# Optimization experiments

Measured on AMD Instinct MI355X. Metric: run time of the kernel, lower is better.

The kernel has to match this reference:

```python
import jax, jax.numpy as jnp
import numpy as np

B = 8192
H_IN = 128
H = 512
Z = 128
N = 512   # must equal H due to W_up(h,h) -> W_down(n,.) chaining in the source
RW = 16
TEMP = 0.666
EPS = 1e-20


def _xavier(key, shape):
    fan_in, fan_out = shape[0], shape[1]
    lim = float(np.sqrt(6.0 / (fan_in + fan_out)))
    return jax.random.uniform(key, shape, jnp.float32, -lim, lim)


def setup_inputs() -> dict:
    key = jax.random.key(0)
    ks = jax.random.split(key, 24)
    inp = {
        'latent': jax.random.normal(ks[0], (B, Z), jnp.float32),
        'inputs': jnp.zeros((B, H_IN), jnp.float32),
        'gumbel_u': jax.random.uniform(ks[1], (RW, B, N), jnp.float32),
        # weights stored [in, out] for x @ W
        'W_int': _xavier(ks[2], (Z, H)),   'b_int': jnp.zeros((H,), jnp.float32),
        'W_intl': _xavier(ks[3], (Z, H)),  'b_intl': jnp.zeros((H,), jnp.float32),
        'W_hup': _xavier(ks[4], (H, H)),   'b_hup': jnp.zeros((H,), jnp.float32),
        'W_cup': _xavier(ks[5], (H, H)),   'b_cup': jnp.zeros((H,), jnp.float32),
        'W_hupl': _xavier(ks[6], (H, H)),  'b_hupl': jnp.zeros((H,), jnp.float32),
        'W_cupl': _xavier(ks[7], (H, H)),  'b_cupl': jnp.zeros((H,), jnp.float32),
        'W_lstm': _xavier(ks[8], (H_IN + H, 4 * H)), 'b_lstm': jnp.zeros((4 * H,), jnp.float32),
        'W_up': _xavier(ks[9], (H, H)),    'b_up': jnp.zeros((H,), jnp.float32),
        'W_down': _xavier(ks[10], (N, H_IN)),        # no bias
        'W_downl': _xavier(ks[11], (N, H_IN)),       # no bias
        'W_outl': _xavier(ks[12], (H, 1)), 'b_outl': jnp.zeros((1,), jnp.float32),
    }
    return inp


def _lstm_step(x, hx, cx, W_lstm, b_lstm):
    gates = jnp.concatenate([x, hx], axis=1) @ W_lstm + b_lstm  # [B, 4H]
    i, g, f, o = jnp.split(gates, 4, axis=1)
    cy = cx * jax.nn.sigmoid(f + 1.0) + jax.nn.sigmoid(i) * jnp.tanh(g)
    hy = jax.nn.sigmoid(o) * jnp.tanh(cy)
    return hy, cy


def _forward(latent, inputs, gumbel_u,
             W_int, b_int, W_intl, b_intl,
             W_hup, b_hup, W_cup, b_cup,
             W_hupl, b_hupl, W_cupl, b_cupl,
             W_lstm, b_lstm, W_up, b_up,
             W_down, W_downl, W_outl, b_outl):
    inter = jnp.tanh(latent @ W_int + b_int)
    hx = jnp.tanh(inter @ W_hup + b_hup)
    cx = jnp.tanh(inter @ W_cup + b_cup)
    inter_l = jnp.tanh(latent @ W_intl + b_intl)
    hxl = jnp.tanh(inter_l @ W_hupl + b_hupl)
    cxl = jnp.tanh(inter_l @ W_cupl + b_cupl)

    def step1(carry, u):
        x, h, c = carry
        hy, cy = _lstm_step(x, h, c, W_lstm, b_lstm)
        logits = hy @ W_up + b_up                       # [B, N]
        g = -jnp.log(-jnp.log(u + EPS) + EPS)           # gumbel noise
        y = jax.nn.softmax((logits + g) / TEMP, axis=1)
        y_hard = (y == jnp.max(y, axis=1, keepdims=True)).astype(y.dtype)
        y = jax.lax.stop_gradient(y_hard - y) + y       # straight-through hard sample
        return (y @ W_down, hy, cy), y

    _, out_steps = jax.lax.scan(step1, (inputs, hx, cx), gumbel_u)  # [RW, B, N]

    def step2(carry, y):
        h, c = carry
        xl = y @ W_downl
        hy, cy = _lstm_step(xl, h, c, W_lstm, b_lstm)   # source reuses lstm_cell here
        return (hy, cy), hy @ W_outl + b_outl           # [B, 1]

    _, line_steps = jax.lax.scan(step2, (hxl, cxl), out_steps)      # [RW, B, 1]

    return (jnp.transpose(out_steps, (1, 0, 2)),   # [B, RW, N]
            jnp.transpose(line_steps, (1, 0, 2)))  # [B, RW, 1]


def reference(latent, inputs, gumbel_u,
              W_int, b_int, W_intl, b_intl,
              W_hup, b_hup, W_cup, b_cup,
              W_hupl, b_hupl, W_cupl, b_cupl,
              W_lstm, b_lstm, W_up, b_up,
              W_down, W_downl, W_outl, b_outl):
    return _forward(latent, inputs, gumbel_u,
                    W_int, b_int, W_intl, b_intl,
                    W_hup, b_hup, W_cup, b_cup,
                    W_hupl, b_hupl, W_cupl, b_cupl,
                    W_lstm, b_lstm, W_up, b_up,
                    W_down, W_downl, W_outl, b_outl)
```

## Files before the change

### kernel.cpp

```cpp
#include <hip/hip_runtime.h>

#define NB 8192
#define NH 512
#define NZ 128
#define NIN 128
#define NN 512
#define NRW 16
#define NG 2048

typedef _Float16 f16;
typedef _Float16 f16x8 __attribute__((ext_vector_type(8)));
typedef float f32x4 __attribute__((ext_vector_type(4)));

__device__ __forceinline__ float sigm(float x) { return 1.0f / (1.0f + expf(-x)); }

__device__ __forceinline__ int oc_of(int c)
{
    return (((c >> 4) & 3) << 9) + ((c >> 6) << 4) + (c & 15);
}
__device__ __forceinline__ int cperm(int j)
{
    return (j & 15) | (((j >> 4) & 31) << 6) | (((j >> 9) & 3) << 4);
}

__device__ __forceinline__ void swz_xcd(int& bx, int& by)
{
    const int gx = gridDim.x;
    const int nwg = gx * gridDim.y;
    int lin = by * gx + bx;
    lin = (lin & 7) * (nwg >> 3) + (lin >> 3);
    const int sh = 31 - __clz(gx);
    bx = lin & (gx - 1);
    by = lin >> sh;
}

__device__ __forceinline__ void gload16(const f16* g, f16* l)
{
    __builtin_amdgcn_global_load_lds(
        (const __attribute__((address_space(1))) void*)g,
        (__attribute__((address_space(3))) void*)l, 16, 0, 0);
}

__device__ __forceinline__ int swz4(int row) { return (row & 3) ^ ((row >> 2) & 3); }

__device__ __forceinline__ void stage_tile(f16* tilebase, const f16* src,
                                           int rowbase, int kb, int wid, int lane)
{
#pragma unroll
    for (int q = 0; q < 2; ++q) {
        const int iw = wid * 2 + q;
        const int chunk = (iw << 6) | lane;
        const int row = chunk >> 2;
        const int p = (chunk & 3) ^ swz4(row);
        const f16* g = src + (size_t)(rowbase + row) * NH + kb + (p << 3);
        gload16(g, tilebase + (iw << 9));
    }
}

__device__ __forceinline__ f16x8 frag(const f16* tile, int row, int sl)
{
    return *(const f16x8*)(tile + row * 32 + ((sl ^ swz4(row)) << 3));
}

__device__ __forceinline__ void readA(f16x8 (&a)[4], const f16* sbuf, int wr, int r16, int sl)
{
#pragma unroll
    for (int f = 0; f < 4; ++f) a[f] = frag(sbuf, wr + f * 16 + r16, sl);
}

__device__ __forceinline__ void loadBfr(f16x8 (&d)[4], const f16* p, size_t base)
{
#pragma unroll
    for (int f = 0; f < 4; ++f) d[f] = *(const f16x8*)(p + base + f * 512);
}

__device__ __forceinline__ f32x4 MM(const f16x8 a, const f16x8 b, f32x4 c)
{
    return __builtin_amdgcn_mfma_f32_16x16x32_f16(a, b, c, 0, 0, 0);
}

template<int SPLIT>
__device__ __forceinline__ void core3(const f16* Ahi, const f16* Alo,
                                      const f16* Bph, const f16* Bpl,
                                      f16* s0h, f16* s0l, f16* s1h, f16* s1l,
                                      int bm, int bnblk, int wid, int lane, int wr, int wc2,
                                      f32x4 (&acc)[4][4])
{
    const int r16 = lane & 15, sl = lane >> 4;
    const size_t bwoff = (size_t)(wc2 << 11) + lane * 8;
    f16x8 bAh[4], bAl[4], bBh[4], bBl[4];

    stage_tile(s0h, Ahi, bm, 0, wid, lane);
    if (SPLIT) stage_tile(s0l, Alo, bm, 0, wid, lane);
    loadBfr(bAh, Bph, (((size_t)bnblk << 4) << 12) + bwoff);
    if (SPLIT) loadBfr(bAl, Bpl, (((size_t)bnblk << 4) << 12) + bwoff);

#pragma unroll 1
    for (int kt = 0; kt < 16; kt += 2) {
        __syncthreads();
        {
            const int kn = kt + 1;
            stage_tile(s1h, Ahi, bm, kn << 5, wid, lane);
            if (SPLIT) stage_tile(s1l, Alo, bm, kn << 5, wid, lane);
            loadBfr(bBh, Bph, ((((size_t)bnblk << 4) + kn) << 12) + bwoff);
            if (SPLIT) loadBfr(bBl, Bpl, ((((size_t)bnblk << 4) + kn) << 12) + bwoff);
        }
        f16x8 ah[4], al[4];
        readA(ah, s0h, wr, r16, sl);
        if (SPLIT) readA(al, s0l, wr, r16, sl);
        __builtin_amdgcn_s_setprio(1);
#pragma unroll
        for (int i = 0; i < 4; ++i)
#pragma unroll
            for (int j = 0; j < 4; ++j) {
                acc[i][j] = MM(ah[i], bAh[j], acc[i][j]);
                if (SPLIT) {
                    acc[i][j] = MM(al[i], bAh[j], acc[i][j]);
                    acc[i][j] = MM(ah[i], bAl[j], acc[i][j]);
                }
            }
        __builtin_amdgcn_s_setprio(0);
        __syncthreads();
        if (kt + 2 < 16) {
            const int kn = kt + 2;
            stage_tile(s0h, Ahi, bm, kn << 5, wid, lane);
            if (SPLIT) stage_tile(s0l, Alo, bm, kn << 5, wid, lane);
            loadBfr(bAh, Bph, ((((size_t)bnblk << 4) + kn) << 12) + bwoff);
            if (SPLIT) loadBfr(bAl, Bpl, ((((size_t)bnblk << 4) + kn) << 12) + bwoff);
        }
        readA(ah, s1h, wr, r16, sl);
        if (SPLIT) readA(al, s1l, wr, r16, sl);
        __builtin_amdgcn_s_setprio(1);
#pragma unroll
        for (int i = 0; i < 4; ++i)
#pragma unroll
            for (int j = 0; j < 4; ++j) {
                acc[i][j] = MM(ah[i], bBh[j], acc[i][j]);
                if (SPLIT) {
                    acc[i][j] = MM(al[i], bBh[j], acc[i][j]);
                    acc[i][j] = MM(ah[i], bBl[j], acc[i][j]);
                }
            }
        __builtin_amdgcn_s_setprio(0);
    }
}

template<int DO_L1, int DO_L2>
__global__ __launch_bounds__(256, 2)
void fused_gate(const f16* __restrict__ a1hi, const f16* __restrict__ a1lo,
                const f16* __restrict__ a2hi,
                const f16* __restrict__ Wlp_hi, const f16* __restrict__ Wlp_lo,
                const float* __restrict__ blp,
                const float* __restrict__ gdown, const float* __restrict__ gdownl,
                const float2* __restrict__ part,
                float* __restrict__ out0, int t_out,
                float* __restrict__ c1, f16* __restrict__ o1hi, f16* __restrict__ o1lo,
                float* __restrict__ c2, f16* __restrict__ o2hi,
                const float* __restrict__ Woutl, float* __restrict__ out1, int t2)
{
    __shared__ f16 s[4][4096];
    __shared__ int winlds[128];
    int bx = blockIdx.x, by = blockIdx.y;
    swz_xcd(bx, by);
    const int bm = by << 7;
    const int tid = threadIdx.x;
    const int wid = tid >> 6, lane = tid & 63;
    const int wr = ((wid >> 1) & 1) << 6;
    const int wc2 = wid & 1;
    const bool isL1 = DO_L1 && (!DO_L2 || blockIdx.z == 0);

    if (part != nullptr && tid < 128) {
        const float2* p = part + (size_t)(bm + tid) * 8;
        float best = -INFINITY;
        int bi = 0x7fffffff;
#pragma unroll
        for (int q = 0; q < 8; ++q) {
            const float2 pv = p[q];
            if (pv.x > best || (pv.x == best && (int)pv.y < bi)) { best = pv.x; bi = (int)pv.y; }
        }
        winlds[tid] = bi;
    }

    f32x4 acc[4][4];
#pragma unroll
    for (int i = 0; i < 4; ++i)
#pragma unroll
        for (int j = 0; j < 4; ++j) acc[i][j] = (f32x4)(0.0f);

    const int m = lane & 15, rg = lane >> 4;
    const int colb = (bx << 7) + (wc2 << 6);
    const int jj = ((colb >> 6) << 4) + m;
    float bi4[4];
#pragma unroll
    for (int g = 0; g < 4; ++g) bi4[g] = blp[colb + g * 16 + m];

    if (isL1) {
        core3<1>(a1hi, a1lo, Wlp_hi, Wlp_lo, s[0], s[1], s[2], s[3],
                 bm, bx, wid, lane, wr, wc2, acc);
#pragma unroll
        for (int i = 0; i < 4; ++i) {
#pragma unroll
            for (int r = 0; r < 4; ++r) {
                const int row = bm + wr + i * 16 + rg * 4 + r;
                float ex[4] = {0.f, 0.f, 0.f, 0.f};
                if (part != nullptr) {
                    const float* exr = gdown + (size_t)winlds[row - bm] * NG;
#pragma unroll
                    for (int g = 0; g < 4; ++g) ex[g] = exr[colb + g * 16 + m];
                }
                const float ig = acc[i][0][r] + bi4[0] + ex[0];
                const float gg = acc[i][1][r] + bi4[1] + ex[1];
                const float fg = acc[i][2][r] + bi4[2] + ex[2];
                const float og = acc[i][3][r] + bi4[3] + ex[3];
                const size_t cidx = (size_t)row * NH + jj;
                const float cx = c1[cidx];
                const float cy = cx * sigm(fg + 1.0f) + sigm(ig) * tanhf(gg);
                const float hy = sigm(og) * tanhf(cy);
                c1[cidx] = cy;
                const f16 a = (f16)hy;
                o1hi[cidx] = a;
                o1lo[cidx] = (f16)(hy - (float)a);
            }
        }
        if (part != nullptr) {
            const int rr = tid >> 1;
            const int cs = (bx << 5) + ((tid & 1) << 4);
            const int win = winlds[rr];
            float* orow = out0 + ((size_t)(bm + rr) * NRW + t_out) * NN + cs;
#pragma unroll
            for (int e = 0; e < 16; e += 4) {
                const int c0 = cs + e;
                *(float4*)(orow + e) = make_float4(c0 == win, c0 + 1 == win, c0 + 2 == win, c0 + 3 == win);
            }
        }
    } else {
        core3<0>(a2hi, nullptr, Wlp_hi, nullptr, s[0], nullptr, s[1], nullptr,
                 bm, bx, wid, lane, wr, wc2, acc);
        const float wout = Woutl[jj];
#pragma unroll
        for (int i = 0; i < 4; ++i) {
#pragma unroll
            for (int r = 0; r < 4; ++r) {
                const int row = bm + wr + i * 16 + rg * 4 + r;
                const float* exr = gdownl + (size_t)winlds[row - bm] * NG;
                float ex[4];
#pragma unroll
                for (int g = 0; g < 4; ++g) ex[g] = exr[colb + g * 16 + m];
                const float ig = acc[i][0][r] + bi4[0] + ex[0];
                const float gg = acc[i][1][r] + bi4[1] + ex[1];
                const float fg = acc[i][2][r] + bi4[2] + ex[2];
                const float og = acc[i][3][r] + bi4[3] + ex[3];
                const size_t cidx = (size_t)row * NH + jj;
                const float cx = c2[cidx];
                const float cy = cx * sigm(fg + 1.0f) + sigm(ig) * tanhf(gg);
                const float hy = sigm(og) * tanhf(cy);
                c2[cidx] = cy;
                o2hi[cidx] = (f16)hy;
                float pt = hy * wout;
#pragma unroll
                for (int msk = 1; msk < 16; msk <<= 1) pt += __shfl_xor(pt, msk);
                if (m == 0) atomicAdd(&out1[(size_t)row * NRW + t2], pt);
            }
        }
        if (!DO_L1) {
            const int rr = tid >> 1;
            const int cs = (bx << 5) + ((tid & 1) << 4);
            const int win = winlds[rr];
            float* orow = out0 + ((size_t)(bm + rr) * NRW + t_out) * NN + cs;
#pragma unroll
            for (int e = 0; e < 16; e += 4) {
                const int c0 = cs + e;
                *(float4*)(orow + e) = make_float4(c0 == win, c0 + 1 == win, c0 + 2 == win, c0 + 3 == win);
            }
        }
    }
}

__global__ __launch_bounds__(256, 2)
void mfma_logits_argmax(const f16* __restrict__ Ahi, const f16* __restrict__ Alo,
                        const f16* __restrict__ Bph, const f16* __restrict__ Bpl,
                        const float* __restrict__ bias,
                        const float* __restrict__ gu,
                        float2* __restrict__ part, int t)
{
    __shared__ f16 s[4][4096];
    int bx = blockIdx.x, by = blockIdx.y;
    swz_xcd(bx, by);
    const int bm = by << 7;
    const int tid = threadIdx.x;
    const int wid = tid >> 6, lane = tid & 63;
    const int wr = ((wid >> 1) & 1) << 6;
    const int wc2 = wid & 1;

    f32x4 acc[4][4];
#pragma unroll
    for (int i = 0; i < 4; ++i)
#pragma unroll
        for (int j = 0; j < 4; ++j) acc[i][j] = (f32x4)(0.0f);

    core3<1>(Ahi, Alo, Bph, Bpl, s[0], s[1], s[2], s[3], bm, bx, wid, lane, wr, wc2, acc);

    const int r16 = lane & 15, rg = lane >> 4;
    const int cb = (bx << 1) + wc2;
    float bi[4];
#pragma unroll
    for (int j = 0; j < 4; ++j) bi[j] = bias[(bx << 7) + (wc2 << 6) + j * 16 + r16];

#pragma unroll
    for (int i = 0; i < 4; ++i) {
#pragma unroll
        for (int r = 0; r < 4; ++r) {
            const int row = bm + wr + i * 16 + rg * 4 + r;
            const float* urow = gu + ((size_t)t * NB + row) * NN;
            float best = -INFINITY;
            int bidx = 0x7fffffff;
#pragma unroll
            for (int j = 0; j < 4; ++j) {
                const int col = (bx << 7) + (wc2 << 6) + j * 16 + r16;
                const float u = urow[col];
                const float g = -logf(-logf(u + 1e-20f) + 1e-20f);
                const float v = acc[i][j][r] + bi[j] + g;
                if (v > best || (v == best && col < bidx)) { best = v; bidx = col; }
            }
#pragma unroll
            for (int msk = 1; msk < 16; msk <<= 1) {
                const float ov = __shfl_xor(best, msk);
                const int oi = __shfl_xor(bidx, msk);
                if (ov > best || (ov == best && oi < bidx)) { best = ov; bidx = oi; }
            }
            if (r16 == 0) part[(size_t)row * 8 + cb] = make_float2(best, (float)bidx);
        }
    }
}

__global__ __launch_bounds__(256, 2)
void init4(const f16* __restrict__ i1hi, const f16* __restrict__ i1lo,
           const f16* __restrict__ i2hi, const f16* __restrict__ i2lo,
           const f16* __restrict__ Whp_hi, const f16* __restrict__ Whp_lo,
           const f16* __restrict__ Wcp_hi, const f16* __restrict__ Wcp_lo,
           const f16* __restrict__ Whlp_hi, const f16* __restrict__ Whlp_lo,
           const f16* __restrict__ Wclp_hi, const f16* __restrict__ Wclp_lo,
           const float* __restrict__ b_hup, const float* __restrict__ b_cup,
           const float* __restrict__ b_hupl, const float* __restrict__ b_cupl,
           float* __restrict__ c1, float* __restrict__ c2,
           f16* __restrict__ h1hi, f16* __restrict__ h1lo, f16* __restrict__ h2hi)
{
    __shared__ f16 s[4][4096];
    const int z = blockIdx.z;
    const f16 *Ahi, *Alo, *Bh, *Bl;
    const float* bias;
    switch (z) {
        case 0: Ahi = i1hi; Alo = i1lo; Bh = Whp_hi;  Bl = Whp_lo;  bias = b_hup;  break;
        case 1: Ahi = i1hi; Alo = i1lo; Bh = Wcp_hi;  Bl = Wcp_lo;  bias = b_cup;  break;
        case 2: Ahi = i2hi; Alo = i2lo; Bh = Whlp_hi; Bl = Whlp_lo; bias = b_hupl; break;
        default: Ahi = i2hi; Alo = i2lo; Bh = Wclp_hi; Bl = Wclp_lo; bias = b_cupl; break;
    }
    int bx = blockIdx.x, by = blockIdx.y;
    swz_xcd(bx, by);
    const int bm = by << 7;
    const int tid = threadIdx.x;
    const int wid = tid >> 6, lane = tid & 63;
    const int wr = ((wid >> 1) & 1) << 6;
    const int wc2 = wid & 1;

    f32x4 acc[4][4];
#pragma unroll
    for (int i = 0; i < 4; ++i)
#pragma unroll
        for (int j = 0; j < 4; ++j) acc[i][j] = (f32x4)(0.0f);

    core3<1>(Ahi, Alo, Bh, Bl, s[0], s[1], s[2], s[3], bm, bx, wid, lane, wr, wc2, acc);

    const int r16 = lane & 15, rg = lane >> 4;
#pragma unroll
    for (int i = 0; i < 4; ++i) {
#pragma unroll
        for (int r = 0; r < 4; ++r) {
            const int row = bm + wr + i * 16 + rg * 4 + r;
#pragma unroll
            for (int j = 0; j < 4; ++j) {
                const int col = (bx << 7) + (wc2 << 6) + j * 16 + r16;
                float v = tanhf(acc[i][j][r] + bias[col]);
                const size_t idx = (size_t)row * NH + col;
                if (z == 0) {
                    const f16 a = (f16)v;
                    h1hi[idx] = a;
                    h1lo[idx] = (f16)(v - (float)a);
                } else if (z == 1) c1[idx] = v;
                else if (z == 2) h2hi[idx] = (f16)v;
                else c2[idx] = v;
            }
        }
    }
}

__global__ __launch_bounds__(256)
void gemm128_split(const float* __restrict__ A,
                   const float* __restrict__ W0, const float* __restrict__ b0,
                   const float* __restrict__ W1, const float* __restrict__ b1,
                   f16* __restrict__ o0hi, f16* __restrict__ o0lo,
                   f16* __restrict__ o1hi, f16* __restrict__ o1lo)
{
    const float* W = blockIdx.z ? W1 : W0;
    const float* bias = blockIdx.z ? b1 : b0;
    f16* ohi = blockIdx.z ? o1hi : o0hi;
    f16* olo = blockIdx.z ? o1lo : o0lo;
    __shared__ float As[16][128];
    __shared__ float Bs[16][128];
    const int bm = blockIdx.y << 7, bn = blockIdx.x << 7;
    const int tid = threadIdx.x;
    const int tx = tid & 15, ty = tid >> 4;
    const int sar = tid >> 1, sac = (tid & 1) << 3;
    const int sbk = tid >> 4, sbc = (tid & 15) << 3;
    float acc[2][2][4][4] = {};
    const float* Ap = A + (size_t)(bm + sar) * NZ + sac;
    const float* Wp = W + (size_t)sbk * NH + bn + sbc;
    for (int kb = 0; kb < NZ; kb += 16) {
        const float4 av0 = *(const float4*)(Ap + kb);
        const float4 av1 = *(const float4*)(Ap + kb + 4);
        const float4 bv0 = *(const float4*)(Wp + (size_t)kb * NH);
        const float4 bv1 = *(const float4*)(Wp + (size_t)kb * NH + 4);
        __syncthreads();
        As[sac + 0][sar] = av0.x; As[sac + 1][sar] = av0.y;
        As[sac + 2][sar] = av0.z; As[sac + 3][sar] = av0.w;
        As[sac + 4][sar] = av1.x; As[sac + 5][sar] = av1.y;
        As[sac + 6][sar] = av1.z; As[sac + 7][sar] = av1.w;
        *(float4*)&Bs[sbk][sbc] = bv0;
        *(float4*)&Bs[sbk][sbc + 4] = bv1;
        __syncthreads();
#pragma unroll
        for (int kk = 0; kk < 16; ++kk) {
            float a[2][4], b[2][4];
            *(float4*)a[0] = *(const float4*)&As[kk][ty << 2];
            *(float4*)a[1] = *(const float4*)&As[kk][64 + (ty << 2)];
            *(float4*)b[0] = *(const float4*)&Bs[kk][tx << 2];
            *(float4*)b[1] = *(const float4*)&Bs[kk][64 + (tx << 2)];
#pragma unroll
            for (int rh = 0; rh < 2; ++rh)
#pragma unroll
                for (int ch = 0; ch < 2; ++ch)
#pragma unroll
                    for (int i = 0; i < 4; ++i)
#pragma unroll
                        for (int j = 0; j < 4; ++j)
                            acc[rh][ch][i][j] = fmaf(a[rh][i], b[ch][j], acc[rh][ch][i][j]);
        }
    }
    float4 bi4[2];
    bi4[0] = *(const float4*)(bias + bn + (tx << 2));
    bi4[1] = *(const float4*)(bias + bn + 64 + (tx << 2));
    const float bia[2][4] = {{bi4[0].x, bi4[0].y, bi4[0].z, bi4[0].w},
                             {bi4[1].x, bi4[1].y, bi4[1].z, bi4[1].w}};
#pragma unroll
    for (int rh = 0; rh < 2; ++rh)
#pragma unroll
        for (int i = 0; i < 4; ++i) {
            const int row = bm + rh * 64 + (ty << 2) + i;
#pragma unroll
            for (int ch = 0; ch < 2; ++ch) {
                const int col = bn + ch * 64 + (tx << 2);
#pragma unroll
                for (int j = 0; j < 4; ++j) {
                    const float v = tanhf(acc[rh][ch][i][j] + bia[ch][j]);
                    const size_t idx = (size_t)row * NH + col + j;
                    const f16 a = (f16)v;
                    ohi[idx] = a;
                    olo[idx] = (f16)(v - (float)a);
                }
            }
        }
}

__global__ __launch_bounds__(256)
void gemm128_gdown(const float* __restrict__ A0, const float* __restrict__ A1,
                   const float* __restrict__ W,
                   float* __restrict__ C0, float* __restrict__ C1)
{
    const float* A = blockIdx.z ? A1 : A0;
    float* C = blockIdx.z ? C1 : C0;
    __shared__ float As[16][128];
    __shared__ float Bs[16][128];
    const int bm = blockIdx.y << 7, bn = blockIdx.x << 7;
    const int tid = threadIdx.x;
    const int tx = tid & 15, ty = tid >> 4;
    const int sar = tid >> 1, sac = (tid & 1) << 3;
    const int sbk = tid >> 4, sbc = (tid & 15) << 3;
    float acc[2][2][4][4] = {};
    const float* Ap = A + (size_t)(bm + sar) * NIN + sac;
    const float* Wp = W + (size_t)sbk * NG + bn + sbc;
    for (int kb = 0; kb < NIN; kb += 16) {
        const float4 av0 = *(const float4*)(Ap + kb);
        const float4 av1 = *(const float4*)(Ap + kb + 4);
        const float4 bv0 = *(const float4*)(Wp + (size_t)kb * NG);
        const float4 bv1 = *(const float4*)(Wp + (size_t)kb * NG + 4);
        __syncthreads();
        As[sac + 0][sar] = av0.x; As[sac + 1][sar] = av0.y;
        As[sac + 2][sar] = av0.z; As[sac + 3][sar] = av0.w;
        As[sac + 4][sar] = av1.x; As[sac + 5][sar] = av1.y;
        As[sac + 6][sar] = av1.z; As[sac + 7][sar] = av1.w;
        *(float4*)&Bs[sbk][sbc] = bv0;
        *(float4*)&Bs[sbk][sbc + 4] = bv1;
        __syncthreads();
#pragma unroll
        for (int kk = 0; kk < 16; ++kk) {
            float a[2][4], b[2][4];
            *(float4*)a[0] = *(const float4*)&As[kk][ty << 2];
            *(float4*)a[1] = *(const float4*)&As[kk][64 + (ty << 2)];
            *(float4*)b[0] = *(const float4*)&Bs[kk][tx << 2];
            *(float4*)b[1] = *(const float4*)&Bs[kk][64 + (tx << 2)];
#pragma unroll
            for (int rh = 0; rh < 2; ++rh)
#pragma unroll
                for (int ch = 0; ch < 2; ++ch)
#pragma unroll
                    for (int i = 0; i < 4; ++i)
#pragma unroll
                        for (int j = 0; j < 4; ++j)
                            acc[rh][ch][i][j] = fmaf(a[rh][i], b[ch][j], acc[rh][ch][i][j]);
        }
    }
#pragma unroll
    for (int rh = 0; rh < 2; ++rh)
#pragma unroll
        for (int i = 0; i < 4; ++i) {
            const int row = bm + rh * 64 + (ty << 2) + i;
#pragma unroll
            for (int ch = 0; ch < 2; ++ch) {
                const int col = bn + ch * 64 + (tx << 2);
                *(float4*)(C + (size_t)row * NG + cperm(col)) =
                    make_float4(acc[rh][ch][i][0], acc[rh][ch][i][1],
                                acc[rh][ch][i][2], acc[rh][ch][i][3]);
            }
        }
}

__global__ __launch_bounds__(256)
void tsplit_pack_all(const float* __restrict__ Wl, const float* __restrict__ Wup,
                     const float* __restrict__ Whp, const float* __restrict__ Wcp,
                     const float* __restrict__ Whlp, const float* __restrict__ Wclp,
                     f16* __restrict__ Wlp_hi, f16* __restrict__ Wlp_lo,
                     f16* __restrict__ Wup_hi, f16* __restrict__ Wup_lo,
                     f16* __restrict__ Whp_hi, f16* __restrict__ Whp_lo,
                     f16* __restrict__ Wcp_hi, f16* __restrict__ Wcp_lo,
                     f16* __restrict__ Whlp_hi, f16* __restrict__ Whlp_lo,
                     f16* __restrict__ Wclp_hi, f16* __restrict__ Wclp_lo)
{
    const int z = blockIdx.z;
    const int nblkcnt = (z == 0) ? 16 : 4;
    if ((int)blockIdx.y >= nblkcnt) return;
    const float* src;
    int ldin, perm;
    f16 *ph, *pl;
    switch (z) {
        case 0: src = Wl;   ldin = NG; perm = 1; ph = Wlp_hi;  pl = Wlp_lo;  break;
        case 1: src = Wup;  ldin = NH; perm = 0; ph = Wup_hi;  pl = Wup_lo;  break;
        case 2: src = Whp;  ldin = NH; perm = 0; ph = Whp_hi;  pl = Whp_lo;  break;
        case 3: src = Wcp;  ldin = NH; perm = 0; ph = Wcp_hi;  pl = Wcp_lo;  break;
        case 4: src = Whlp; ldin = NH; perm = 0; ph = Whlp_hi; pl = Whlp_lo; break;
        default: src = Wclp; ldin = NH; perm = 0; ph = Wclp_hi; pl = Wclp_lo; break;
    }
    const int kt = blockIdx.x;
    const int nblk = blockIdx.y;
#pragma unroll
    for (int q = 0; q < 2; ++q) {
        const int cch = threadIdx.x + q * 256;
        const int wc2 = cch >> 8, f = (cch >> 6) & 3, slc = (cch >> 4) & 3, r16 = cch & 15;
        const int n = (nblk << 7) + (wc2 << 6) + (f << 4) + r16;
        const int ncol = perm ? oc_of(n) : n;
        const int k0 = (kt << 5) + (slc << 3);
        f16x8 h8, l8;
#pragma unroll
        for (int e = 0; e < 8; ++e) {
            const float v = src[(size_t)(k0 + e) * ldin + ncol];
            const f16 hi = (f16)v;
            h8[e] = hi;
            l8[e] = (f16)(v - (float)hi);
        }
        const size_t off = ((((size_t)nblk << 4) + kt) << 12) + (size_t)cch * 8;
        *(f16x8*)(ph + off) = h8;
        *(f16x8*)(pl + off) = l8;
    }
}

__global__ __launch_bounds__(256)
void permb(const float* __restrict__ b, float* __restrict__ bp)
{
    const int c = blockIdx.x * 256 + threadIdx.x;
    bp[c] = b[oc_of(c)];
}

__global__ __launch_bounds__(256)
void out1_init(float* __restrict__ out1, const float* __restrict__ boutl)
{
    const size_t i = (size_t)blockIdx.x * 256 + threadIdx.x;
    out1[i] = boutl[0];
}

extern "C" void kernel_launch(void* const* d_in, const int* in_sizes, int n_in,
                              void* d_out, int out_size, void* d_ws, size_t ws_size,
                              hipStream_t stream)
{
    const float* latent  = (const float*)d_in[0];
    const float* gu      = (const float*)d_in[2];
    const float* W_int   = (const float*)d_in[3];
    const float* b_int   = (const float*)d_in[4];
    const float* W_intl  = (const float*)d_in[5];
    const float* b_intl  = (const float*)d_in[6];
    const float* W_hup   = (const float*)d_in[7];
    const float* b_hup   = (const float*)d_in[8];
    const float* W_cup   = (const float*)d_in[9];
    const float* b_cup   = (const float*)d_in[10];
    const float* W_hupl  = (const float*)d_in[11];
    const float* b_hupl  = (const float*)d_in[12];
    const float* W_cupl  = (const float*)d_in[13];
    const float* b_cupl  = (const float*)d_in[14];
    const float* W_lstm  = (const float*)d_in[15];
    const float* b_lstm  = (const float*)d_in[16];
    const float* W_up    = (const float*)d_in[17];
    const float* b_up    = (const float*)d_in[18];
    const float* W_down  = (const float*)d_in[19];
    const float* W_downl = (const float*)d_in[20];
    const float* W_outl  = (const float*)d_in[21];
    const float* b_outl  = (const float*)d_in[22];

    float* out0 = (float*)d_out;
    float* out1 = out0 + (size_t)NB * NRW * NN;

    float* ws     = (float*)d_ws;
    float* c1     = ws;
    float* c2     = c1 + (size_t)NB * NH;
    float* gdown  = c2 + (size_t)NB * NH;
    float* gdownl = gdown + (size_t)NN * NG;
    float* blp    = gdownl + (size_t)NN * NG;
    float2* part  = (float2*)(blp + NG);
    f16* fp = (f16*)(part + (size_t)NB * 8);
    f16* h1hi[2]; f16* h1lo[2]; f16* h2hi[2];
    h1hi[0] = fp;                    fp += (size_t)NB * NH;
    h1lo[0] = fp;                    fp += (size_t)NB * NH;
    h1hi[1] = fp;                    fp += (size_t)NB * NH;
    h1lo[1] = fp;                    fp += (size_t)NB * NH;
    h2hi[0] = fp;                    fp += (size_t)NB * NH;
    h2hi[1] = fp;                    fp += (size_t)NB * NH;
    f16* i1hi = fp;                  fp += (size_t)NB * NH;
    f16* i1lo = fp;                  fp += (size_t)NB * NH;
    f16* i2hi = fp;                  fp += (size_t)NB * NH;
    f16* i2lo = fp;                  fp += (size_t)NB * NH;
    f16* Wlp_hi = fp;                fp += (size_t)NG * NH;
    f16* Wlp_lo = fp;                fp += (size_t)NG * NH;
    f16* Wup_hi = fp;                fp += (size_t)NN * NH;
    f16* Wup_lo = fp;                fp += (size_t)NN * NH;
    f16* Whp_hi = fp;                fp += (size_t)NH * NH;
    f16* Whp_lo = fp;                fp += (size_t)NH * NH;
    f16* Wcp_hi = fp;                fp += (size_t)NH * NH;
    f16* Wcp_lo = fp;                fp += (size_t)NH * NH;
    f16* Whlp_hi = fp;               fp += (size_t)NH * NH;
    f16* Whlp_lo = fp;               fp += (size_t)NH * NH;
    f16* Wclp_hi = fp;               fp += (size_t)NH * NH;
    f16* Wclp_lo = fp;               fp += (size_t)NH * NH;

    const dim3 blk(256);

    tsplit_pack_all<<<dim3(16, 16, 6), blk, 0, stream>>>(
        W_lstm + (size_t)NIN * NG, W_up, W_hup, W_cup, W_hupl, W_cupl,
        Wlp_hi, Wlp_lo, Wup_hi, Wup_lo, Whp_hi, Whp_lo, Wcp_hi, Wcp_lo,
        Whlp_hi, Whlp_lo, Wclp_hi, Wclp_lo);
    permb<<<dim3(NG / 256), blk, 0, stream>>>(b_lstm, blp);
    gemm128_gdown<<<dim3(NG / 128, NN / 128, 2), blk, 0, stream>>>(W_down, W_downl, W_lstm,
                                                                   gdown, gdownl);
    gemm128_split<<<dim3(NH / 128, NB / 128, 2), blk, 0, stream>>>(latent, W_int, b_int,
                                                                   W_intl, b_intl,
                                                                   i1hi, i1lo, i2hi, i2lo);
    init4<<<dim3(NH / 128, NB / 128, 4), blk, 0, stream>>>(
        i1hi, i1lo, i2hi, i2lo,
        Whp_hi, Whp_lo, Wcp_hi, Wcp_lo, Whlp_hi, Whlp_lo, Wclp_hi, Wclp_lo,
        b_hup, b_cup, b_hupl, b_cupl,
        c1, c2, h1hi[0], h1lo[0], h2hi[0]);
    out1_init<<<dim3(NB * NRW / 256), blk, 0, stream>>>(out1, b_outl);

    const dim3 g1(NG / 128, NB / 128, 1);
    const dim3 g2(NG / 128, NB / 128, 2);
    const dim3 gl(NN / 128, NB / 128);

    fused_gate<1, 0><<<g1, blk, 0, stream>>>(h1hi[0], h1lo[0], nullptr,
                                             Wlp_hi, Wlp_lo, blp, gdown, gdownl,
                                             nullptr, out0, 0,
                                             c1, h1hi[1], h1lo[1],
                                             nullptr, nullptr, nullptr, nullptr, 0);
    mfma_logits_argmax<<<gl, blk, 0, stream>>>(h1hi[1], h1lo[1], Wup_hi, Wup_lo,
                                               b_up, gu, part, 0);

    int c1i = 1, c2i = 0;
    for (int t = 0; t < NRW - 1; ++t) {
        const int n1 = c1i ^ 1, n2 = c2i ^ 1;
        fused_gate<1, 1><<<g2, blk, 0, stream>>>(h1hi[c1i], h1lo[c1i], h2hi[c2i],
                                                 Wlp_hi, Wlp_lo, blp, gdown, gdownl,
                                                 part, out0, t,
                                                 c1, h1hi[n1], h1lo[n1],
                                                 c2, h2hi[n2], W_outl, out1, t);
        mfma_logits_argmax<<<gl, blk, 0, stream>>>(h1hi[n1], h1lo[n1], Wup_hi, Wup_lo,
                                                   b_up, gu, part, t + 1);
        c1i = n1;
        c2i = n2;
    }
    fused_gate<0, 1><<<g1, blk, 0, stream>>>(nullptr, nullptr, h2hi[c2i],
                                             Wlp_hi, Wlp_lo, blp, gdown, gdownl,
                                             part, out0, NRW - 1,
                                             nullptr, nullptr, nullptr,
                                             c2, h2hi[c2i ^ 1], W_outl, out1, NRW - 1);
}
```

Baseline: 2.759 ms.

## Replace per-step kernel launches with a cooperative persistent kernel using grid syncs

After: 5.469 ms. 98.2% more time.

```diff
diff --git a/kernel.cpp b/kernel.cpp
--- a/kernel.cpp
+++ b/kernel.cpp
@@ -1,4 +1,7 @@
 #include <hip/hip_runtime.h>
+#include <hip/hip_cooperative_groups.h>
+
+namespace cg = cooperative_groups;
 
 #define NB 8192
 #define NH 512
@@ -23,12 +26,17 @@
     return (j & 15) | (((j >> 4) & 31) << 6) | (((j >> 9) & 3) << 4);
 }
 
+__device__ __forceinline__ int swz_lin(int lin, int nwg)
+{
+    return (lin & 7) * (nwg >> 3) + (lin >> 3);
+}
+
 __device__ __forceinline__ void swz_xcd(int& bx, int& by)
 {
     const int gx = gridDim.x;
     const int nwg = gx * gridDim.y;
     int lin = by * gx + bx;
-    lin = (lin & 7) * (nwg >> 3) + (lin >> 3);
+    lin = swz_lin(lin, nwg);
     const int sh = 31 - __clz(gx);
     bx = lin & (gx - 1);
     by = lin >> sh;
@@ -145,47 +153,61 @@
     }
 }
 
-template<int DO_L1, int DO_L2>
-__global__ __launch_bounds__(256, 2)
-void fused_gate(const f16* __restrict__ a1hi, const f16* __restrict__ a1lo,
-                const f16* __restrict__ a2hi,
-                const f16* __restrict__ Wlp_hi, const f16* __restrict__ Wlp_lo,
-                const float* __restrict__ blp,
-                const float* __restrict__ gdown, const float* __restrict__ gdownl,
-                const float2* __restrict__ part,
-                float* __restrict__ out0, int t_out,
-                float* __restrict__ c1, f16* __restrict__ o1hi, f16* __restrict__ o1lo,
-                float* __restrict__ c2, f16* __restrict__ o2hi,
-                const float* __restrict__ Woutl, float* __restrict__ out1, int t2)
-{
-    __shared__ f16 s[4][4096];
-    __shared__ int winlds[128];
-    int bx = blockIdx.x, by = blockIdx.y;
-    swz_xcd(bx, by);
+__device__ __forceinline__ void gather_win(int* winlds, const float2* part, int bm)
+{
+    const int tid = threadIdx.x;
+    if (tid < 128) {
+        const float2* p = part + (size_t)(bm + tid) * 8;
+        float best = -INFINITY;
+        int bi = 0x7fffffff;
+#pragma unroll
+        for (int q = 0; q < 8; ++q) {
+            const float2 pv = p[q];
+            if (pv.x > best || (pv.x == best && (int)pv.y < bi)) { best = pv.x; bi = (int)pv.y; }
+        }
+        winlds[tid] = bi;
+    }
+}
+
+__device__ __forceinline__ void write_onehot(float* out0, int bm, int bx, int t_out,
+                                             const int* winlds)
+{
+    const int tid = threadIdx.x;
+    const int rr = tid >> 1;
+    const int cs = (bx << 5) + ((tid & 1) << 4);
+    const int win = winlds[rr];
+    float* orow = out0 + ((size_t)(bm + rr) * NRW + t_out) * NN + cs;
+#pragma unroll
+    for (int e = 0; e < 16; e += 4) {
+        const int c0 = cs + e;
+        *(float4*)(orow + e) = make_float4(c0 == win, c0 + 1 == win, c0 + 2 == win, c0 + 3 == win);
+    }
+}
+
+template<int HAS_PART>
+__device__ __forceinline__ void job_gate1(f16 (*s)[4096], int* winlds, int bx, int by,
+                                          const f16* a1hi, const f16* a1lo,
+                                          const f16* Wlp_hi, const f16* Wlp_lo,
+                                          const float* blp, const float* gdown,
+                                          const float2* part,
+                                          float* out0, int t_out,
+                                          float* c1, f16* o1hi, f16* o1lo)
+{
     const int bm = by << 7;
     const int tid = threadIdx.x;
     const int wid = tid >> 6, lane = tid & 63;
     const int wr = ((wid >> 1) & 1) << 6;
     const int wc2 = wid & 1;
-    const bool isL1 = DO_L1 && (!DO_L2 || blockIdx.z == 0);
-
-    if (part != nullptr && tid < 128) {
-        const float2* p = part + (size_t)(bm + tid) * 8;
-        float best = -INFINITY;
-        int bi = 0x7fffffff;
-#pragma unroll
-        for (int q = 0; q < 8; ++q) {
-            const float2 pv = p[q];
-            if (pv.x > best || (pv.x == best && (int)pv.y < bi)) { best = pv.x; bi = (int)pv.y; }
-        }
-        winlds[tid] = bi;
-    }
+    __syncthreads();
+    if (HAS_PART) gather_win(winlds, part, bm);
 
     f32x4 acc[4][4];
 #pragma unroll
     for (int i = 0; i < 4; ++i)
 #pragma unroll
         for (int j = 0; j < 4; ++j) acc[i][j] = (f32x4)(0.0f);
+
+    core3<1>(a1hi, a1lo, Wlp_hi, Wlp_lo, s[0], s[1], s[2], s[3], bm, bx, wid, lane, wr, wc2, acc);
 
     const int m = lane & 15, rg = lane >> 4;
     const int colb = (bx << 7) + (wc2 << 6);
@@ -194,103 +216,108 @@
 #pragma unroll
     for (int g = 0; g < 4; ++g) bi4[g] = blp[colb + g * 16 + m];
 
-    if (isL1) {
-        core3<1>(a1hi, a1lo, Wlp_hi, Wlp_lo, s[0], s[1], s[2], s[3],
-                 bm, bx, wid, lane, wr, wc2, acc);
-#pragma unroll
-        for (int i = 0; i < 4; ++i) {
-#pragma unroll
-            for (int r = 0; r < 4; ++r) {
-                const int row = bm + wr + i * 16 + rg * 4 + r;
-                float ex[4] = {0.f, 0.f, 0.f, 0.f};
-                if (part != nullptr) {
-                    const float* exr = gdown + (size_t)winlds[row - bm] * NG;
-#pragma unroll
-                    for (int g = 0; g < 4; ++g) ex[g] = exr[colb + g * 16 + m];
-                }
-                const float ig = acc[i][0][r] + bi4[0] + ex[0];
-                const float gg = acc[i][1][r] + bi4[1] + ex[1];
-                const float fg = acc[i][2][r] + bi4[2] + ex[2];
-                const float og = acc[i][3][r] + bi4[3] + ex[3];
-                const size_t cidx = (size_t)row * NH + jj;
-                const float cx = c1[cidx];
-                const float cy = cx * sigm(fg + 1.0f) + sigm(ig) * tanhf(gg);
-                const float hy = sigm(og) * tanhf(cy);
-                c1[cidx] = cy;
-                const f16 a = (f16)hy;
-                o1hi[cidx] = a;
-                o1lo[cidx] = (f16)(hy - (float)a);
+#pragma unroll
+    for (int i = 0; i < 4; ++i) {
+#pragma unroll
+        for (int r = 0; r < 4; ++r) {
+            const int row = bm + wr + i * 16 + rg * 4 + r;
+            float ex[4] = {0.f, 0.f, 0.f, 0.f};
+            if (HAS_PART) {
+                const float* exr = gdown + (size_t)winlds[row - bm] * NG;
+#pragma unroll
+                for (int g = 0; g < 4; ++g) ex[g] = exr[colb + g * 16 + m];
             }
-        }
-        if (part != nullptr) {
-            const int rr = tid >> 1;
-            const int cs = (bx << 5) + ((tid & 1) << 4);
-            const int win = winlds[rr];
-            float* orow = out0 + ((size_t)(bm + rr) * NRW + t_out) * NN + cs;
-#pragma unroll
-            for (int e = 0; e < 16; e += 4) {
-                const int c0 = cs + e;
-                *(float4*)(orow + e) = make_float4(c0 == win, c0 + 1 == win, c0 + 2 == win, c0 + 3 == win);
-            }
-        }
-    } else {
-        core3<0>(a2hi, nullptr, Wlp_hi, nullptr, s[0], nullptr, s[1], nullptr,
-                 bm, bx, wid, lane, wr, wc2, acc);
-        const float wout = Woutl[jj];
-#pragma unroll
-        for (int i = 0; i < 4; ++i) {
-#pragma unroll
-            for (int r = 0; r < 4; ++r) {
-                const int row = bm + wr + i * 16 + rg * 4 + r;
-                const float* exr = gdownl + (size_t)winlds[row - bm] * NG;
-                float ex[4];
-#pragma unroll
-                for (int g = 0; g < 4; ++g) ex[g] = exr[colb + g * 16 + m];
-                const float ig = acc[i][0][r] + bi4[0] + ex[0];
-                const float gg = acc[i][1][r] + bi4[1] + ex[1];
-                const float fg = acc[i][2][r] + bi4[2] + ex[2];
-                const float og = acc[i][3][r] + bi4[3] + ex[3];
-                const size_t cidx = (size_t)row * NH + jj;
-                const float cx = c2[cidx];
-                const float cy = cx * sigm(fg + 1.0f) + sigm(ig) * tanhf(gg);
-                const float hy = sigm(og) * tanhf(cy);
-                c2[cidx] = cy;
-                o2hi[cidx] = (f16)hy;
-                float pt = hy * wout;
-#pragma unroll
-                for (int msk = 1; msk < 16; msk <<= 1) pt += __shfl_xor(pt, msk);
-                if (m == 0) atomicAdd(&out1[(size_t)row * NRW + t2], pt);
-            }
-        }
-        if (!DO_L1) {
-            const int rr = tid >> 1;
-            const int cs = (bx << 5) + ((tid & 1) << 4);
-            const int win = winlds[rr];
-            float* orow = out0 + ((size_t)(bm + rr) * NRW + t_out) * NN + cs;
-#pragma unroll
-            for (int e = 0; e < 16; e += 4) {
-                const int c0 = cs + e;
-                *(float4*)(orow + e) = make_float4(c0 == win, c0 + 1 == win, c0 + 2 == win, c0 + 3 == win);
-            }
-        }
-    }
-}
-
-__global__ __launch_bounds__(256, 2)
-void mfma_logits_argmax(const f16* __restrict__ Ahi, const f16* __restrict__ Alo,
-                        const f16* __restrict__ Bph, const f16* __restrict__ Bpl,
-                        const float* __restrict__ bias,
-                        const float* __restrict__ gu,
-                        float2* __restrict__ part, int t)
-{
-    __shared__ f16 s[4][4096];
-    int bx = blockIdx.x, by = blockIdx.y;
-    swz_xcd(bx, by);
+            const float ig = acc[i][0][r] + bi4[0] + ex[0];
+            const float gg = acc[i][1][r] + bi4[1] + ex[1];
+            const float fg = acc[i][2][r] + bi4[2] + ex[2];
+            const float og = acc[i][3][r] + bi4[3] + ex[3];
+            const size_t cidx = (size_t)row * NH + jj;
+            const float cx = c1[cidx];
+            const float cy = cx * sigm(fg + 1.0f) + sigm(ig) * tanhf(gg);
+            const float hy = sigm(og) * tanhf(cy);
+            c1[cidx] = cy;
+            const f16 a = (f16)hy;
+            o1hi[cidx] = a;
+            o1lo[cidx] = (f16)(hy - (float)a);
+        }
+    }
+    if (HAS_PART) write_onehot(out0, bm, bx, t_out, winlds);
+}
+
+template<int WRITE_OUT0>
+__device__ __forceinline__ void job_gate2(f16 (*s)[4096], int* winlds, int bx, int by,
+                                          const f16* a2hi, const f16* Wlp_hi,
+                                          const float* blp, const float* gdownl,
+                                          const float2* part,
+                                          float* out0, int t_out,
+                                          float* c2, f16* o2hi,
+                                          const float* Woutl, float* out1, int t2)
+{
     const int bm = by << 7;
     const int tid = threadIdx.x;
     const int wid = tid >> 6, lane = tid & 63;
     const int wr = ((wid >> 1) & 1) << 6;
     const int wc2 = wid & 1;
+    __syncthreads();
+    gather_win(winlds, part, bm);
+
+    f32x4 acc[4][4];
+#pragma unroll
+    for (int i = 0; i < 4; ++i)
+#pragma unroll
+        for (int j = 0; j < 4; ++j) acc[i][j] = (f32x4)(0.0f);
+
+    core3<0>(a2hi, nullptr, Wlp_hi, nullptr, s[0], nullptr, s[1], nullptr,
+             bm, bx, wid, lane, wr, wc2, acc);
+
+    const int m = lane & 15, rg = lane >> 4;
+    const int colb = (bx << 7) + (wc2 << 6);
+    const int jj = ((colb >> 6) << 4) + m;
+    const float wout = Woutl[jj];
+    float bi4[4];
+#pragma unroll
+    for (int g = 0; g < 4; ++g) bi4[g] = blp[colb + g * 16 + m];
+
+#pragma unroll
+    for (int i = 0; i < 4; ++i) {
+#pragma unroll
+        for (int r = 0; r < 4; ++r) {
+            const int row = bm + wr + i * 16 + rg * 4 + r;
+            const float* exr = gdownl + (size_t)winlds[row - bm] * NG;
+            float ex[4];
+#pragma unroll
+            for (int g = 0; g < 4; ++g) ex[g] = exr[colb + g * 16 + m];
+            const float ig = acc[i][0][r] + bi4[0] + ex[0];
+            const float gg = acc[i][1][r] + bi4[1] + ex[1];
+            const float fg = acc[i][2][r] + bi4[2] + ex[2];
+            const float og = acc[i][3][r] + bi4[3] + ex[3];
+            const size_t cidx = (size_t)row * NH + jj;
+            const float cx = c2[cidx];
+            const float cy = cx * sigm(fg + 1.0f) + sigm(ig) * tanhf(gg);
+            const float hy = sigm(og) * tanhf(cy);
+            c2[cidx] = cy;
+            o2hi[cidx] = (f16)hy;
+            float pt = hy * wout;
+#pragma unroll
+            for (int msk = 1; msk < 16; msk <<= 1) pt += __shfl_xor(pt, msk);
+            if (m == 0) atomicAdd(&out1[(size_t)row * NRW + t2], pt);
+        }
+    }
+    if (WRITE_OUT0) write_onehot(out0, bm, bx, t_out, winlds);
+}
+
+__device__ __forceinline__ void job_logits(f16 (*s)[4096], int bx, int by,
+                                           const f16* Ahi, const f16* Alo,
+                                           const f16* Bph, const f16* Bpl,
+                                           const float* bias, const float* gu,
+                                           float2* part, int t)
+{
+    const int bm = by << 7;
+    const int tid = threadIdx.x;
+    const int wid = tid >> 6, lane = tid & 63;
+    const int wr = ((wid >> 1) & 1) << 6;
+    const int wc2 = wid & 1;
+    __syncthreads();
 
     f32x4 acc[4][4];
 #pragma unroll
@@ -331,6 +358,107 @@
             if (r16 == 0) part[(size_t)row * 8 + cb] = make_float2(best, (float)bidx);
         }
     }
+}
+
+__global__ __launch_bounds__(256, 2)
+void persist_loop(const f16* __restrict__ Wlp_hi, const f16* __restrict__ Wlp_lo,
+                  const f16* __restrict__ Wup_hi, const f16* __restrict__ Wup_lo,
+                  const float* __restrict__ blp, const float* __restrict__ bup,
+                  const float* __restrict__ gdown, const float* __restrict__ gdownl,
+                  const float* __restrict__ gu, const float* __restrict__ Woutl,
+                  float2* __restrict__ part, float* __restrict__ out0,
+                  float* __restrict__ out1,
+                  float* __restrict__ c1, float* __restrict__ c2,
+                  f16* h1hi0, f16* h1lo0, f16* h1hi1, f16* h1lo1,
+                  f16* h2hi0, f16* h2hi1)
+{
+    cg::grid_group grid = cg::this_grid();
+    __shared__ f16 s[4][4096];
+    __shared__ int winlds[128];
+    f16* h1hi[2] = {h1hi0, h1hi1};
+    f16* h1lo[2] = {h1lo0, h1lo1};
+    f16* h2hi[2] = {h2hi0, h2hi1};
+
+    for (int t = 0; t <= NRW; ++t) {
+        const int nL1 = (t < NRW) ? 1024 : 0;
+        const int nTot = nL1 + ((t >= 1) ? 1024 : 0);
+        for (int job = blockIdx.x; job < nTot; job += gridDim.x) {
+            const bool isL1 = job < nL1;
+            const int tile = isL1 ? job : (job - nL1);
+            const int lin = swz_lin(tile, 1024);
+            const int bx = lin & 15, by = lin >> 4;
+            if (isL1) {
+                if (t == 0)
+                    job_gate1<0>(s, winlds, bx, by, h1hi[0], h1lo[0], Wlp_hi, Wlp_lo,
+                                 blp, gdown, nullptr, out0, 0, c1, h1hi[1], h1lo[1]);
+                else
+                    job_gate1<1>(s, winlds, bx, by, h1hi[t & 1], h1lo[t & 1], Wlp_hi, Wlp_lo,
+                                 blp, gdown, part, out0, t - 1,
+                                 c1, h1hi[(t + 1) & 1], h1lo[(t + 1) & 1]);
+            } else {
+                const int s2 = t - 1;
+                if (t == NRW)
+                    job_gate2<1>(s, winlds, bx, by, h2hi[s2 & 1], Wlp_hi, blp, gdownl, part,
+                                 out0, NRW - 1, c2, h2hi[(s2 + 1) & 1], Woutl, out1, s2);
+                else
+                    job_gate2<0>(s, winlds, bx, by, h2hi[s2 & 1], Wlp_hi, blp, gdownl, part,
+                                 out0, 0, c2, h2hi[(s2 + 1) & 1], Woutl, out1, s2);
+            }
+        }
+        grid.sync();
+        if (t == NRW) break;
+        for (int job = blockIdx.x; job < 256; job += gridDim.x) {
+            const int lin = swz_lin(job, 256);
+            const int bx = lin & 3, by = lin >> 2;
+            job_logits(s, bx, by, h1hi[(t + 1) & 1], h1lo[(t + 1) & 1],
+                       Wup_hi, Wup_lo, bup, gu, part, t);
+        }
+        grid.sync();
+    }
+}
+
+template<int DO_L1, int DO_L2>
+__global__ __launch_bounds__(256, 2)
+void fused_gate_fb(const f16* a1hi, const f16* a1lo, const f16* a2hi,
+                   const f16* Wlp_hi, const f16* Wlp_lo, const float* blp,
+                   const float* gdown, const float* gdownl,
+                   const float2* part, float* out0, int t_out,
+                   float* c1, f16* o1hi, f16* o1lo,
+                   float* c2, f16* o2hi,
+                   const float* Woutl, float* out1, int t2)
+{
+    __shared__ f16 s[4][4096];
+    __shared__ int winlds[128];
+    int lin = blockIdx.y * 16 + blockIdx.x;
+    lin = swz_lin(lin, 1024);
+    const int bx = lin & 15, by = lin >> 4;
+    const bool isL1 = DO_L1 && (!DO_L2 || blockIdx.z == 0);
+    if (isL1) {
+        if (part)
+            job_gate1<1>(s, winlds, bx, by, a1hi, a1lo, Wlp_hi, Wlp_lo, blp, gdown,
+                         part, out0, t_out, c1, o1hi, o1lo);
+        else
+            job_gate1<0>(s, winlds, bx, by, a1hi, a1lo, Wlp_hi, Wlp_lo, blp, gdown,
+                         nullptr, out0, 0, c1, o1hi, o1lo);
+    } else {
+        if (DO_L1)
+            job_gate2<0>(s, winlds, bx, by, a2hi, Wlp_hi, blp, gdownl, part,
+                         out0, t_out, c2, o2hi, Woutl, out1, t2);
+        else
+            job_gate2<1>(s, winlds, bx, by, a2hi, Wlp_hi, blp, gdownl, part,
+                         out0, t_out, c2, o2hi, Woutl, out1, t2);
+    }
+}
+
+__global__ __launch_bounds__(256, 2)
+void logits_fb(const f16* Ahi, const f16* Alo, const f16* Bph, const f16* Bpl,
+               const float* bias, const float* gu, float2* part, int t)
+{
+    __shared__ f16 s[4][4096];
+    int lin = blockIdx.y * 4 + blockIdx.x;
+    lin = swz_lin(lin, 256);
+    const int bx = lin & 3, by = lin >> 2;
+    job_logits(s, bx, by, Ahi, Alo, Bph, Bpl, bias, gu, part, t);
 }
 
 __global__ __launch_bounds__(256, 2)
@@ -634,13 +762,12 @@
     float* blp    = gdownl + (size_t)NN * NG;
     float2* part  = (float2*)(blp + NG);
     f16* fp = (f16*)(part + (size_t)NB * 8);
-    f16* h1hi[2]; f16* h1lo[2]; f16* h2hi[2];
-    h1hi[0] = fp;                    fp += (size_t)NB * NH;
-    h1lo[0] = fp;                    fp += (size_t)NB * NH;
-    h1hi[1] = fp;                    fp += (size_t)NB * NH;
-    h1lo[1] = fp;                    fp += (size_t)NB * NH;
-    h2hi[0] = fp;                    fp += (size_t)NB * NH;
-    h2hi[1] = fp;                    fp += (size_t)NB * NH;
+    f16* h1hi0 = fp;                 fp += (size_t)NB * NH;
+    f16* h1lo0 = fp;                 fp += (size_t)NB * NH;
+    f16* h1hi1 = fp;                 fp += (size_t)NB * NH;
+    f16* h1lo1 = fp;                 fp += (size_t)NB * NH;
+    f16* h2hi0 = fp;                 fp += (size_t)NB * NH;
+    f16* h2hi1 = fp;                 fp += (size_t)NB * NH;
     f16* i1hi = fp;                  fp += (size_t)NB * NH;
     f16* i1lo = fp;                  fp += (size_t)NB * NH;
     f16* i2hi = fp;                  fp += (size_t)NB * NH;
@@ -674,37 +801,57 @@
         i1hi, i1lo, i2hi, i2lo,
         Whp_hi, Whp_lo, Wcp_hi, Wcp_lo, Whlp_hi, Whlp_lo, Wclp_hi, Wclp_lo,
         b_hup, b_cup, b_hupl, b_cupl,
-        c1, c2, h1hi[0], h1lo[0], h2hi[0]);
+        c1, c2, h1hi0, h1lo0, h2hi0);
     out1_init<<<dim3(NB * NRW / 256), blk, 0, stream>>>(out1, b_outl);
 
-    const dim3 g1(NG / 128, NB / 128, 1);
-    const dim3 g2(NG / 128, NB / 128, 2);
-    const dim3 gl(NN / 128, NB / 128);
-
-    fused_gate<1, 0><<<g1, blk, 0, stream>>>(h1hi[0], h1lo[0], nullptr,
-                                             Wlp_hi, Wlp_lo, blp, gdown, gdownl,
-                                             nullptr, out0, 0,
-                                             c1, h1hi[1], h1lo[1],
-                                             nullptr, nullptr, nullptr, nullptr, 0);
-    mfma_logits_argmax<<<gl, blk, 0, stream>>>(h1hi[1], h1lo[1], Wup_hi, Wup_lo,
-                                               b_up, gu, part, 0);
-
-    int c1i = 1, c2i = 0;
-    for (int t = 0; t < NRW - 1; ++t) {
-        const int n1 = c1i ^ 1, n2 = c2i ^ 1;
-        fused_gate<1, 1><<<g2, blk, 0, stream>>>(h1hi[c1i], h1lo[c1i], h2hi[c2i],
-                                                 Wlp_hi, Wlp_lo, blp, gdown, gdownl,
-                                                 part, out0, t,
-                                                 c1, h1hi[n1], h1lo[n1],
-                                                 c2, h2hi[n2], W_outl, out1, t);
-        mfma_logits_argmax<<<gl, blk, 0, stream>>>(h1hi[n1], h1lo[n1], Wup_hi, Wup_lo,
-                                                   b_up, gu, part, t + 1);
-        c1i = n1;
-        c2i = n2;
-    }
-    fused_gate<0, 1><<<g1, blk, 0, stream>>>(nullptr, nullptr, h2hi[c2i],
-                                             Wlp_hi, Wlp_lo, blp, gdown, gdownl,
-                                             part, out0, NRW - 1,
-                                             nullptr, nullptr, nullptr,
-                                             c2, h2hi[c2i ^ 1], W_outl, out1, NRW - 1);
-}
+    int maxb = 0;
+    hipOccupancyMaxActiveBlocksPerMultiprocessor(&maxb, persist_loop, 256, 0);
+    if (maxb < 1) maxb = 1;
+    if (maxb > 2) maxb = 2;
+    const int nblk_coop = maxb * 256;
+
+    void* cargs[] = {
+        (void*)&Wlp_hi, (void*)&Wlp_lo, (void*)&Wup_hi, (void*)&Wup_lo,
+        (void*)&blp, (void*)&b_up, (void*)&gdown, (void*)&gdownl,
+        (void*)&gu, (void*)&W_outl,
+        (void*)&part, (void*)&out0, (void*)&out1,
+        (void*)&c1, (void*)&c2,
+        (void*)&h1hi0, (void*)&h1lo0, (void*)&h1hi1, (void*)&h1lo1,
+        (void*)&h2hi0, (void*)&h2hi1};
+
+    hipError_t ce = hipLaunchCooperativeKernel(persist_loop, dim3(nblk_coop), blk,
+                                               cargs, 0u, stream);
+    if (ce != hipSuccess) {
+        (void)hipGetLastError();
+        f16* h1hiA[2] = {h1hi0, h1hi1};
+        f16* h1loA[2] = {h1lo0, h1lo1};
+        f16* h2hiA[2] = {h2hi0, h2hi1};
+        const dim3 g1(16, 64, 1), g2(16, 64, 2), gl(4, 64);
+
+        fused_gate_fb<1, 0><<<g1, blk, 0, stream>>>(h1hiA[0], h1loA[0], nullptr,
+                                                    Wlp_hi, Wlp_lo, blp, gdown, gdownl,
+                                                    nullptr, out0, 0,
+                                                    c1, h1hiA[1], h1loA[1],
+                                                    nullptr, nullptr, W_outl, out1, 0);
+        logits_fb<<<gl, blk, 0, stream>>>(h1hiA[1], h1loA[1], Wup_hi, Wup_lo,
+                                          b_up, gu, part, 0);
+        int c1i = 1, c2i = 0;
+        for (int t = 0; t < NRW - 1; ++t) {
+            const int n1 = c1i ^ 1, n2 = c2i ^ 1;
+            fused_gate_fb<1, 1><<<g2, blk, 0, stream>>>(h1hiA[c1i], h1loA[c1i], h2hiA[c2i],
+                                                        Wlp_hi, Wlp_lo, blp, gdown, gdownl,
+                                                        part, out0, t,
+                                                        c1, h1hiA[n1], h1loA[n1],
+                                                        c2, h2hiA[n2], W_outl, out1, t);
+            logits_fb<<<gl, blk, 0, stream>>>(h1hiA[n1], h1loA[n1], Wup_hi, Wup_lo,
+                                              b_up, gu, part, t + 1);
+            c1i = n1;
+            c2i = n2;
+        }
+        fused_gate_fb<0, 1><<<g1, blk, 0, stream>>>(nullptr, nullptr, h2hiA[c2i],
+                                                    Wlp_hi, Wlp_lo, blp, gdown, gdownl,
+                                                    part, out0, NRW - 1,
+                                                    nullptr, nullptr, nullptr,
+                                                    c2, h2hiA[c2i ^ 1], W_outl, out1, NRW - 1);
+    }
+}
```
